# Optimization experiments

Hardware: AMD Instinct MI355X
Metric: run time of the kernel (lower is better)

## Reference

```python
import jax, jax.numpy as jnp
import numpy as np

N_NODES = 50000


def gcn_conv(x, src, dst, W, b, n_nodes):
    """PyG-style GCNConv: x' = D^-1/2 (A + I) D^-1/2 (x W) + b.
    src/dst already include self-loops."""
    h = x @ W  # [N, C_out]
    # symmetric normalization from degree (with self-loops, unit edge weight)
    deg = jax.ops.segment_sum(jnp.ones_like(dst, dtype=h.dtype), dst,
                              num_segments=n_nodes)  # [N]
    dinv = jnp.where(deg > 0, jax.lax.rsqrt(deg), 0.0)
    norm = dinv[src] * dinv[dst]  # [E]
    msg = h[src] * norm[:, None]  # gather + scale, [E, C_out]
    out = jax.ops.segment_sum(msg, dst, num_segments=n_nodes)  # scatter-add
    return out + b


def setup_inputs() -> dict:
    key = jax.random.key(0)
    k1, k2, k3, k4, k5, k6 = jax.random.split(key, 6)
    in_c, hid_c, out_c = 128, 64, 64
    x = jax.random.normal(k1, (N_NODES, in_c), dtype=jnp.float32)
    edge_index = jax.random.randint(k2, (2, 800000), 0, N_NODES, dtype=jnp.int64)
    # Glorot-ish init for weights, zeros for bias (as PyG default)
    W1 = jax.random.normal(k3, (in_c, hid_c), dtype=jnp.float32) / np.sqrt(in_c)
    b1 = jnp.zeros((hid_c,), dtype=jnp.float32)
    W2 = jax.random.normal(k4, (hid_c, out_c), dtype=jnp.float32) / np.sqrt(hid_c)
    b2 = jnp.zeros((out_c,), dtype=jnp.float32)
    return {"x": x, "edge_index": edge_index, "W1": W1, "b1": b1,
            "W2": W2, "b2": b2}


def reference(x, edge_index, W1, b1, W2, b2):
    n = x.shape[0]
    loops = jnp.arange(n, dtype=edge_index.dtype)
    src = jnp.concatenate([edge_index[0], loops])  # add self-loops
    dst = jnp.concatenate([edge_index[1], loops])
    h = gcn_conv(x, src, dst, W1, b1, n)
    h = jax.nn.relu(h)
    return gcn_conv(h, src, dst, W2, b2, n)
```

## Files before the change

kernel.cpp:

```cpp
#include <hip/hip_runtime.h>
#include <hip/hip_fp16.h>


#define C_HID 64
#define NCHUNK 512
#define ES3 768
#define ES4 768

static inline size_t alignup(size_t x) { return (x + 255) & ~(size_t)255; }

typedef __attribute__((address_space(3))) unsigned int lds_uint;
typedef __attribute__((address_space(1))) const unsigned int glob_uint;
typedef __attribute__((ext_vector_type(4))) _Float16 half4;
typedef __attribute__((ext_vector_type(4))) float floatx4;

__device__ __forceinline__ int blockScanIncl256(int v, int* wsum) {
    const int lane = threadIdx.x & 63, wav = threadIdx.x >> 6;
    int s = v;
#pragma unroll
    for (int off = 1; off < 64; off <<= 1) {
        int t = __shfl_up(s, off);
        if (lane >= off) s += t;
    }
    if (lane == 63) wsum[wav] = s;
    __syncthreads();
    if (wav == 0 && lane < 4) {
        int ws = wsum[lane];
#pragma unroll
        for (int off = 1; off < 4; off <<= 1) {
            int t = __shfl_up(ws, off);
            if (lane >= off) ws += t;
        }
        wsum[lane] = ws;
    }
    __syncthreads();
    return (wav ? wsum[wav - 1] : 0) + s;
}

__global__ __launch_bounds__(256) void cvt_w1t_kernel(
    const float* __restrict__ W, __half* __restrict__ Wh) {
    int i = blockIdx.x * 256 + threadIdx.x;
    if (i < 64 * 128) {
        int c = i >> 7, k = i & 127;
        int ks = k ^ ((c & 7) << 3);
        Wh[c * 128 + ks] = __float2half(W[k * 64 + c]);
    }
}

template <int K>
__global__ __launch_bounds__(256) void gemm1_hist_kernel(
    const float* __restrict__ X, const __half* __restrict__ Wh,
    const int* __restrict__ dst, __half* __restrict__ outh,
    int* __restrict__ S, int n, int E, int ePer, int nb) {
    constexpr int XP = K + 8;
    __shared__ __half Xs[64 * XP];
    __shared__ __half WsT[64 * K];
    __shared__ int h[1024];
    const int t = threadIdx.x;
    const int lane = t & 63;
    const int wav = t >> 6;

    if ((int)blockIdx.x < NCHUNK) {
        for (int i = t; i < nb; i += 256) h[i] = 0;
        __syncthreads();
        int beg = blockIdx.x * ePer, end = min(E, beg + ePer);
        for (int e = beg + t; e < end; e += 256)
            atomicAdd(&h[dst[e] >> 6], 1);
        __syncthreads();
        for (int b = t; b < nb; b += 256)
            S[(size_t)b * NCHUNK + blockIdx.x] = h[b];
        return;
    }

    const int row0 = ((int)blockIdx.x - NCHUNK) * 64;
    {
        const char* gb = (const char*)Wh;
        char* lb = (char*)WsT;
        for (int off = wav * 1024; off < K * 64 * 2; off += 4096)
            __builtin_amdgcn_global_load_lds((glob_uint*)(gb + off + lane * 16),
                                             (lds_uint*)(lb + off), 16, 0, 0);
    }
    if (row0 + 64 <= n) {
        const float4* g4 = (const float4*)(X + (size_t)row0 * K);
        for (int i = t; i < 64 * (K / 4); i += 256) {
            float4 v = g4[i];
            int r = i / (K / 4), k0 = (i % (K / 4)) * 4;
            float2 st;
            ((__half2*)&st)[0] = __floats2half2_rn(v.x, v.y);
            ((__half2*)&st)[1] = __floats2half2_rn(v.z, v.w);
            *(float2*)&Xs[r * XP + k0] = st;
        }
    } else {
        for (int i = t; i < 64 * K; i += 256) {
            int r = i / K, k = i % K;
            float xv = (row0 + r < n) ? X[(size_t)(row0 + r) * K + k] : 0.0f;
            Xs[r * XP + k] = __float2half(xv);
        }
    }
    __syncthreads();

    const int rl = lane & 15;
    const int kq = lane >> 4;
    floatx4 acc0 = {0.f, 0.f, 0.f, 0.f};
    floatx4 acc1 = {0.f, 0.f, 0.f, 0.f};
    floatx4 acc2 = {0.f, 0.f, 0.f, 0.f};
    floatx4 acc3 = {0.f, 0.f, 0.f, 0.f};
    const __half* xrow = &Xs[(wav * 16 + rl) * XP];
#pragma unroll
    for (int kb = 0; kb < K / 16; ++kb) {
        const int ka = kb * 16 + kq * 4;
        half4 a = *(const half4*)&xrow[ka];
        {   int col = 0 * 16 + rl;
            half4 b = *(const half4*)&WsT[col * K + (ka ^ ((col & 7) << 3))];
            acc0 = __builtin_amdgcn_mfma_f32_16x16x16f16(a, b, acc0, 0, 0, 0); }
        {   int col = 1 * 16 + rl;
            half4 b = *(const half4*)&WsT[col * K + (ka ^ ((col & 7) << 3))];
            acc1 = __builtin_amdgcn_mfma_f32_16x16x16f16(a, b, acc1, 0, 0, 0); }
        {   int col = 2 * 16 + rl;
            half4 b = *(const half4*)&WsT[col * K + (ka ^ ((col & 7) << 3))];
            acc2 = __builtin_amdgcn_mfma_f32_16x16x16f16(a, b, acc2, 0, 0, 0); }
        {   int col = 3 * 16 + rl;
            half4 b = *(const half4*)&WsT[col * K + (ka ^ ((col & 7) << 3))];
            acc3 = __builtin_amdgcn_mfma_f32_16x16x16f16(a, b, acc3, 0, 0, 0); }
    }
#pragma unroll
    for (int r = 0; r < 4; ++r) {
        int row = row0 + wav * 16 + kq * 4 + r;
        if (row < n) {
            __half* orow = &outh[(size_t)row * 64];
            orow[0 * 16 + rl] = __float2half(acc0[r]);
            orow[1 * 16 + rl] = __float2half(acc1[r]);
            orow[2 * 16 + rl] = __float2half(acc2[r]);
            orow[3 * 16 + rl] = __float2half(acc3[r]);
        }
    }
}

__global__ __launch_bounds__(256) void scan_rows_kernel(
    int* __restrict__ S, int* __restrict__ T) {
    __shared__ int wsum[4];
    const int b = blockIdx.x, t = threadIdx.x;
    int4 v = make_int4(0, 0, 0, 0);
    if (t < NCHUNK / 4) v = ((const int4*)(S + (size_t)b * NCHUNK))[t];
    int p1 = v.x + v.y, p2 = p1 + v.z, p3 = p2 + v.w;
    int incl = blockScanIncl256(p3, wsum);
    int excl = incl - p3;
    if (t < NCHUNK / 4) {
        int4 o;
        o.x = excl; o.y = excl + v.x; o.z = excl + p1; o.w = excl + p2;
        ((int4*)(S + (size_t)b * NCHUNK))[t] = o;
    }
    if (t == 0) T[b] = wsum[3];
}

__global__ __launch_bounds__(256) void scatter_kernel(
    const int* __restrict__ src, const int* __restrict__ dst, int E, int ePer,
    const int* __restrict__ S, const int* __restrict__ T,
    unsigned* __restrict__ ebuf, int nb) {
    __shared__ int tmp[1024];
    __shared__ int arr[1024];
    __shared__ int wsum[4];
    const int b = blockIdx.x, t = threadIdx.x;
    {
        int a0 = (4 * t + 0 < nb) ? T[4 * t + 0] : 0;
        int a1 = (4 * t + 1 < nb) ? T[4 * t + 1] : 0;
        int a2 = (4 * t + 2 < nb) ? T[4 * t + 2] : 0;
        int a3 = (4 * t + 3 < nb) ? T[4 * t + 3] : 0;
        int p1 = a0 + a1, p2 = p1 + a2, p3 = p2 + a3;
        int incl = blockScanIncl256(p3, wsum);
        int excl = incl - p3;
        tmp[4 * t + 0] = excl;
        tmp[4 * t + 1] = excl + a0;
        tmp[4 * t + 2] = excl + p1;
        tmp[4 * t + 3] = excl + p2;
    }
    __syncthreads();
    for (int i = t; i < nb; i += 256)
        arr[i] = S[(size_t)i * NCHUNK + b] + tmp[i];
    __syncthreads();
    int beg = b * ePer, end = min(E, beg + ePer);
    for (int e = beg + t; e < end; e += 256) {
        int d = dst[e];
        int s = src[e];
        int pos = atomicAdd(&arr[d >> 6], 1);
        ebuf[pos] = ((unsigned)s << 6) | (unsigned)(d & 63);
    }
}

__global__ __launch_bounds__(256) void build_kernel(
    const unsigned* __restrict__ ebuf, const int* __restrict__ T,
    int* __restrict__ row_ptr, float* __restrict__ dinv,
    int* __restrict__ esrc, __half* __restrict__ g1, int n, int nb) {
    __shared__ int tmp[1024];
    __shared__ int cnt[64];
    __shared__ int cur[64];
    __shared__ float dvs[64];
    __shared__ int wsum[4];
    const int b = blockIdx.x, t = threadIdx.x;
    {
        int a0 = (4 * t + 0 < nb) ? T[4 * t + 0] : 0;
        int a1 = (4 * t + 1 < nb) ? T[4 * t + 1] : 0;
        int a2 = (4 * t + 2 < nb) ? T[4 * t + 2] : 0;
        int a3 = (4 * t + 3 < nb) ? T[4 * t + 3] : 0;
        int p1 = a0 + a1, p2 = p1 + a2, p3 = p2 + a3;
        int incl = blockScanIncl256(p3, wsum);
        int excl = incl - p3;
        tmp[4 * t + 0] = excl + a0;
        tmp[4 * t + 1] = excl + p1;
        tmp[4 * t + 2] = excl + p2;
        tmp[4 * t + 3] = excl + p3;
    }
    if (t < 64) cnt[t] = 0;
    __syncthreads();
    const int ebeg = b ? tmp[b - 1] : 0;
    const int eend = tmp[b];

    for (int e = ebeg + t; e < eend; e += 256)
        atomicAdd(&cnt[ebuf[e] & 63], 1);
    __syncthreads();
    if (t < 64) {
        int deg = cnt[t];
        int s = deg;
#pragma unroll
        for (int off = 1; off < 64; off <<= 1) {
            int x = __shfl_up(s, off);
            if (t >= off) s += x;
        }
        cur[t] = ebeg + s - deg;
        float dv = rsqrtf(1.0f + (float)deg);
        dvs[t] = dv;
        int v = (b << 6) + t;
        if (v < n) {
            row_ptr[v + 1] = ebeg + s;
            dinv[v] = dv;
            if (v == 0) row_ptr[0] = 0;
        }
    }
    __syncthreads();
    for (int e = ebeg + t; e < eend; e += 256) {
        unsigned p = ebuf[e];
        int pos = atomicAdd(&cur[p & 63], 1);
        esrc[pos] = (int)(p >> 6);
    }
    {
        const int row = t >> 2, q = t & 3;
        const int v = (b << 6) + row;
        if (v < n) {
            float dv = dvs[row];
            float4* gp = (float4*)(g1 + (size_t)v * 64 + q * 16);
            float4 r0 = gp[0], r1 = gp[1];
            __half2* h0 = (__half2*)&r0;
            __half2* h1 = (__half2*)&r1;
#pragma unroll
            for (int i2 = 0; i2 < 4; ++i2) {
                float2 f0 = __half22float2(h0[i2]);
                float2 f1 = __half22float2(h1[i2]);
                h0[i2] = __floats2half2_rn(f0.x * dv, f0.y * dv);
                h1[i2] = __floats2half2_rn(f1.x * dv, f1.y * dv);
            }
            gp[0] = r0;
            gp[1] = r1;
        }
    }
}

__device__ __forceinline__ void addf4(float acc[8], const float4& r) {
    const __half2* h = (const __half2*)&r;
#pragma unroll
    for (int q = 0; q < 4; ++q) {
        float2 f = __half22float2(h[q]);
        acc[2 * q] += f.x;
        acc[2 * q + 1] += f.y;
    }
}

template <bool LDSE>
__device__ __forceinline__ void agg8_body(
    const float4* __restrict__ hs4, const int* es, const int* __restrict__ esg,
    int beg0, int beg, int end, int c8, float acc[8]) {
    int j = beg;
    for (; j + 8 <= end; j += 8) {
        int s0, s1, s2, s3, s4, s5, s6, s7;
        if (LDSE) {
            s0 = es[j];     s1 = es[j + 1]; s2 = es[j + 2]; s3 = es[j + 3];
            s4 = es[j + 4]; s5 = es[j + 5]; s6 = es[j + 6]; s7 = es[j + 7];
        } else {
            const int* p = esg + beg0 + j;
            s0 = p[0]; s1 = p[1]; s2 = p[2]; s3 = p[3];
            s4 = p[4]; s5 = p[5]; s6 = p[6]; s7 = p[7];
        }
        float4 r0 = hs4[(size_t)s0 * 8 + c8];
        float4 r1 = hs4[(size_t)s1 * 8 + c8];
        float4 r2 = hs4[(size_t)s2 * 8 + c8];
        float4 r3 = hs4[(size_t)s3 * 8 + c8];
        float4 r4 = hs4[(size_t)s4 * 8 + c8];
        float4 r5 = hs4[(size_t)s5 * 8 + c8];
        float4 r6 = hs4[(size_t)s6 * 8 + c8];
        float4 r7 = hs4[(size_t)s7 * 8 + c8];
        addf4(acc, r0); addf4(acc, r1); addf4(acc, r2); addf4(acc, r3);
        addf4(acc, r4); addf4(acc, r5); addf4(acc, r6); addf4(acc, r7);
    }
    if (j + 4 <= end) {
        int s0, s1, s2, s3;
        if (LDSE) {
            s0 = es[j]; s1 = es[j + 1]; s2 = es[j + 2]; s3 = es[j + 3];
        } else {
            const int* p = esg + beg0 + j;
            s0 = p[0]; s1 = p[1]; s2 = p[2]; s3 = p[3];
        }
        float4 r0 = hs4[(size_t)s0 * 8 + c8];
        float4 r1 = hs4[(size_t)s1 * 8 + c8];
        float4 r2 = hs4[(size_t)s2 * 8 + c8];
        float4 r3 = hs4[(size_t)s3 * 8 + c8];
        addf4(acc, r0); addf4(acc, r1); addf4(acc, r2); addf4(acc, r3);
        j += 4;
    }
    for (; j < end; ++j) {
        int s0 = LDSE ? es[j] : esg[beg0 + j];
        float4 r0 = hs4[(size_t)s0 * 8 + c8];
        addf4(acc, r0);
    }
}

__global__ __launch_bounds__(256) void agg1_gemm2_kernel(
    const __half* __restrict__ g1, const int* __restrict__ row_ptr,
    const int* __restrict__ esrc, const float* __restrict__ dinv,
    const float* __restrict__ b1, const float* __restrict__ W2,
    __half* __restrict__ g2, int n) {
    __shared__ float Bt[32][68];
    __shared__ float Ws2[64 * 64];
    __shared__ int es[ES3];
    const int t = threadIdx.x, lane = t & 63, wav = t >> 6;
    const int row0 = blockIdx.x * 32;

    const int beg0 = row_ptr[row0];
    const int end0 = row_ptr[min(row0 + 32, n)];
    const int tot = end0 - beg0;
    const bool uselds = (tot <= ES3);
    if (uselds)
        for (int i = t; i < tot; i += 256) es[i] = esrc[beg0 + i];
    __syncthreads();

    {
        const char* gb = (const char*)W2;
        char* lb = (char*)Ws2;
        for (int off = wav * 1024; off < 64 * 64 * 4; off += 4096)
            __builtin_amdgcn_global_load_lds((glob_uint*)(gb + off + lane * 16),
                                             (lds_uint*)(lb + off), 16, 0, 0);
    }

    const int g = t >> 3;
    const int c8 = t & 7;
    const int v = row0 + g;
    const float4* __restrict__ hs4 = (const float4*)g1;

    if (v < n) {
        float acc[8];
        {
            float4 raw = hs4[(size_t)v * 8 + c8];
            const __half2* hp = (const __half2*)&raw;
#pragma unroll
            for (int q = 0; q < 4; ++q) {
                float2 f = __half22float2(hp[q]);
                acc[2 * q] = f.x; acc[2 * q + 1] = f.y;
            }
        }
        const int beg = row_ptr[v] - beg0;
        const int end = row_ptr[v + 1] - beg0;
        if (uselds) agg8_body<true>(hs4, es, esrc, beg0, beg, end, c8, acc);
        else        agg8_body<false>(hs4, es, esrc, beg0, beg, end, c8, acc);
        const float dv0 = dinv[v];
        const float* bb = b1 + c8 * 8;
        float4 w0, w1;
        w0.x = fmaxf(fmaf(acc[0], dv0, bb[0]), 0.f);
        w0.y = fmaxf(fmaf(acc[1], dv0, bb[1]), 0.f);
        w0.z = fmaxf(fmaf(acc[2], dv0, bb[2]), 0.f);
        w0.w = fmaxf(fmaf(acc[3], dv0, bb[3]), 0.f);
        w1.x = fmaxf(fmaf(acc[4], dv0, bb[4]), 0.f);
        w1.y = fmaxf(fmaf(acc[5], dv0, bb[5]), 0.f);
        w1.z = fmaxf(fmaf(acc[6], dv0, bb[6]), 0.f);
        w1.w = fmaxf(fmaf(acc[7], dv0, bb[7]), 0.f);
        *(float4*)&Bt[g][c8 * 8] = w0;
        *(float4*)&Bt[g][c8 * 8 + 4] = w1;
    } else {
        *(float4*)&Bt[g][c8 * 8] = make_float4(0.f, 0.f, 0.f, 0.f);
        *(float4*)&Bt[g][c8 * 8 + 4] = make_float4(0.f, 0.f, 0.f, 0.f);
    }
    __syncthreads();

    const int tx = t & 15;
    const int ty = t >> 4;
    float a2[2][4] = {{0.f}};
#pragma unroll 2
    for (int k0 = 0; k0 < 64; k0 += 4) {
        float4 x0 = *(const float4*)&Bt[2 * ty + 0][k0];
        float4 x1 = *(const float4*)&Bt[2 * ty + 1][k0];
        float4 w0 = *(const float4*)&Ws2[(k0 + 0) * 64 + 4 * tx];
        float4 w1 = *(const float4*)&Ws2[(k0 + 1) * 64 + 4 * tx];
        float4 w2 = *(const float4*)&Ws2[(k0 + 2) * 64 + 4 * tx];
        float4 w3 = *(const float4*)&Ws2[(k0 + 3) * 64 + 4 * tx];
        const float* xp[2] = {(const float*)&x0, (const float*)&x1};
        const float* wp[4] = {(const float*)&w0, (const float*)&w1,
                              (const float*)&w2, (const float*)&w3};
#pragma unroll
        for (int r = 0; r < 2; ++r)
#pragma unroll
            for (int kk = 0; kk < 4; ++kk) {
                float av = xp[r][kk];
#pragma unroll
                for (int cc = 0; cc < 4; ++cc)
                    a2[r][cc] = fmaf(av, wp[kk][cc], a2[r][cc]);
            }
    }
#pragma unroll
    for (int r = 0; r < 2; ++r) {
        int row = row0 + 2 * ty + r;
        if (row < n) {
            float dv = dinv[row];
            __half2 p01 = __floats2half2_rn(a2[r][0] * dv, a2[r][1] * dv);
            __half2 p23 = __floats2half2_rn(a2[r][2] * dv, a2[r][3] * dv);
            float2 st;
            ((__half2*)&st)[0] = p01;
            ((__half2*)&st)[1] = p23;
            *(float2*)&g2[(size_t)row * 64 + 4 * tx] = st;
        }
    }
}

__global__ __launch_bounds__(256) void aggregate2_kernel(
    const __half* __restrict__ hs,
    const int* __restrict__ row_ptr,
    const int* __restrict__ esrc,
    const float* __restrict__ dinv,
    const float* __restrict__ bias,
    float* __restrict__ out, int n) {
    __shared__ int es[ES4];
    const int t = threadIdx.x;
    const int row0 = blockIdx.x * 32;
    const int beg0 = row_ptr[row0];
    const int end0 = row_ptr[min(row0 + 32, n)];
    const int tot = end0 - beg0;
    const bool uselds = (tot <= ES4);
    if (uselds)
        for (int i = t; i < tot; i += 256) es[i] = esrc[beg0 + i];
    __syncthreads();

    const int v = row0 + (t >> 3);
    if (v >= n) return;
    const int c8 = t & 7;
    const float4* __restrict__ hs4 = (const float4*)hs;

    float acc[8];
    {
        float4 raw = hs4[(size_t)v * 8 + c8];
        const __half2* hp = (const __half2*)&raw;
#pragma unroll
        for (int q = 0; q < 4; ++q) {
            float2 f = __half22float2(hp[q]);
            acc[2 * q] = f.x; acc[2 * q + 1] = f.y;
        }
    }

    const int beg = row_ptr[v] - beg0;
    const int end = row_ptr[v + 1] - beg0;
    if (uselds) agg8_body<true>(hs4, es, esrc, beg0, beg, end, c8, acc);
    else        agg8_body<false>(hs4, es, esrc, beg0, beg, end, c8, acc);

    float dv = dinv[v];
    float4 b0 = *(const float4*)(bias + c8 * 8);
    float4 b1v = *(const float4*)(bias + c8 * 8 + 4);
    float4 o0, o1;
    o0.x = fmaf(acc[0], dv, b0.x); o0.y = fmaf(acc[1], dv, b0.y);
    o0.z = fmaf(acc[2], dv, b0.z); o0.w = fmaf(acc[3], dv, b0.w);
    o1.x = fmaf(acc[4], dv, b1v.x); o1.y = fmaf(acc[5], dv, b1v.y);
    o1.z = fmaf(acc[6], dv, b1v.z); o1.w = fmaf(acc[7], dv, b1v.w);
    float4* op = (float4*)(out + (size_t)v * 64 + c8 * 8);
    op[0] = o0;
    op[1] = o1;
}

extern "C" void kernel_launch(void* const* d_in, const int* in_sizes, int n_in,
                              void* d_out, int out_size, void* d_ws, size_t ws_size,
                              hipStream_t stream) {
    const float* x  = (const float*)d_in[0];
    const int*   ei = (const int*)d_in[1];
    const float* W1 = (const float*)d_in[2];
    const float* b1 = (const float*)d_in[3];
    const float* W2 = (const float*)d_in[4];
    const float* b2 = (const float*)d_in[5];
    float* out = (float*)d_out;

    const int C_IN = 128;
    const int n = in_sizes[0] / C_IN;
    const int E = in_sizes[1] / 2;
    const int* src = ei;
    const int* dst = ei + E;

    const int nb = (n + 63) >> 6;
    const int ngb = (n + 63) / 64;
    const int n32 = (n + 31) / 32;
    const int ePer = (E + NCHUNK - 1) / NCHUNK;

    char* w = (char*)d_ws;
    float*    dinv    = (float*)w;    w += alignup((size_t)n * sizeof(float));
    __half*   g1      = (__half*)w;   w += alignup((size_t)n * C_HID * sizeof(__half));
    __half*   g2      = (__half*)w;   w += alignup((size_t)n * C_HID * sizeof(__half));
    int*      row_ptr = (int*)w;      w += alignup((size_t)(n + 1) * sizeof(int));
    int*      S       = (int*)w;      w += alignup((size_t)nb * NCHUNK * sizeof(int));
    int*      T       = (int*)w;      w += alignup((size_t)(nb + 1) * sizeof(int));
    unsigned* ebuf    = (unsigned*)w; w += alignup((size_t)E * sizeof(unsigned));
    int*      esrc    = (int*)w;      w += alignup((size_t)E * sizeof(int));
    __half*   W1h     = (__half*)w;

    cvt_w1t_kernel<<<32, 256, 0, stream>>>(W1, W1h);

    gemm1_hist_kernel<128><<<NCHUNK + ngb, 256, 0, stream>>>(
        x, W1h, dst, g1, S, n, E, ePer, nb);

    scan_rows_kernel<<<nb, 256, 0, stream>>>(S, T);
    scatter_kernel<<<NCHUNK, 256, 0, stream>>>(src, dst, E, ePer, S, T, ebuf, nb);
    build_kernel<<<nb, 256, 0, stream>>>(ebuf, T, row_ptr, dinv, esrc, g1, n, nb);

    agg1_gemm2_kernel<<<n32, 256, 0, stream>>>(
        g1, row_ptr, esrc, dinv, b1, W2, g2, n);

    aggregate2_kernel<<<n32, 256, 0, stream>>>(
        g2, row_ptr, esrc, dinv, b2, out, n);
}
```

Before: 155.1 us.

## Co-schedule GEMM1 with scatter instead of histogram pass

Moves the dense X·W1 MFMA tiles out of the histogram kernel and into the scatter kernel, so the GEMM blocks run alongside the edge scatter instead of the edge histogram. The histogram becomes a lean standalone kernel, and the scatter and GEMM paths share LDS through a union. The aim is to balance work across the two passes and overlap the compute-heavy GEMM with the atomic-heavy scatter. In exchange, the combined kernel's LDS footprint is now the larger of the two layouts, which may reduce occupancy for the scatter blocks.

```diff
diff --git a/kernel.cpp b/kernel.cpp
--- a/kernel.cpp
+++ b/kernel.cpp
@@ -47,93 +47,18 @@
     }
 }
 
-template <int K>
-__global__ __launch_bounds__(256) void gemm1_hist_kernel(
-    const float* __restrict__ X, const __half* __restrict__ Wh,
-    const int* __restrict__ dst, __half* __restrict__ outh,
-    int* __restrict__ S, int n, int E, int ePer, int nb) {
-    constexpr int XP = K + 8;
-    __shared__ __half Xs[64 * XP];
-    __shared__ __half WsT[64 * K];
+__global__ __launch_bounds__(256) void hist_kernel(
+    const int* __restrict__ dst, int* __restrict__ S, int E, int ePer, int nb) {
     __shared__ int h[1024];
     const int t = threadIdx.x;
-    const int lane = t & 63;
-    const int wav = t >> 6;
-
-    if ((int)blockIdx.x < NCHUNK) {
-        for (int i = t; i < nb; i += 256) h[i] = 0;
-        __syncthreads();
-        int beg = blockIdx.x * ePer, end = min(E, beg + ePer);
-        for (int e = beg + t; e < end; e += 256)
-            atomicAdd(&h[dst[e] >> 6], 1);
-        __syncthreads();
-        for (int b = t; b < nb; b += 256)
-            S[(size_t)b * NCHUNK + blockIdx.x] = h[b];
-        return;
-    }
-
-    const int row0 = ((int)blockIdx.x - NCHUNK) * 64;
-    {
-        const char* gb = (const char*)Wh;
-        char* lb = (char*)WsT;
-        for (int off = wav * 1024; off < K * 64 * 2; off += 4096)
-            __builtin_amdgcn_global_load_lds((glob_uint*)(gb + off + lane * 16),
-                                             (lds_uint*)(lb + off), 16, 0, 0);
-    }
-    if (row0 + 64 <= n) {
-        const float4* g4 = (const float4*)(X + (size_t)row0 * K);
-        for (int i = t; i < 64 * (K / 4); i += 256) {
-            float4 v = g4[i];
-            int r = i / (K / 4), k0 = (i % (K / 4)) * 4;
-            float2 st;
-            ((__half2*)&st)[0] = __floats2half2_rn(v.x, v.y);
-            ((__half2*)&st)[1] = __floats2half2_rn(v.z, v.w);
-            *(float2*)&Xs[r * XP + k0] = st;
-        }
-    } else {
-        for (int i = t; i < 64 * K; i += 256) {
-            int r = i / K, k = i % K;
-            float xv = (row0 + r < n) ? X[(size_t)(row0 + r) * K + k] : 0.0f;
-            Xs[r * XP + k] = __float2half(xv);
-        }
-    }
-    __syncthreads();
-
-    const int rl = lane & 15;
-    const int kq = lane >> 4;
-    floatx4 acc0 = {0.f, 0.f, 0.f, 0.f};
-    floatx4 acc1 = {0.f, 0.f, 0.f, 0.f};
-    floatx4 acc2 = {0.f, 0.f, 0.f, 0.f};
-    floatx4 acc3 = {0.f, 0.f, 0.f, 0.f};
-    const __half* xrow = &Xs[(wav * 16 + rl) * XP];
-#pragma unroll
-    for (int kb = 0; kb < K / 16; ++kb) {
-        const int ka = kb * 16 + kq * 4;
-        half4 a = *(const half4*)&xrow[ka];
-        {   int col = 0 * 16 + rl;
-            half4 b = *(const half4*)&WsT[col * K + (ka ^ ((col & 7) << 3))];
-            acc0 = __builtin_amdgcn_mfma_f32_16x16x16f16(a, b, acc0, 0, 0, 0); }
-        {   int col = 1 * 16 + rl;
-            half4 b = *(const half4*)&WsT[col * K + (ka ^ ((col & 7) << 3))];
-            acc1 = __builtin_amdgcn_mfma_f32_16x16x16f16(a, b, acc1, 0, 0, 0); }
-        {   int col = 2 * 16 + rl;
-            half4 b = *(const half4*)&WsT[col * K + (ka ^ ((col & 7) << 3))];
-            acc2 = __builtin_amdgcn_mfma_f32_16x16x16f16(a, b, acc2, 0, 0, 0); }
-        {   int col = 3 * 16 + rl;
-            half4 b = *(const half4*)&WsT[col * K + (ka ^ ((col & 7) << 3))];
-            acc3 = __builtin_amdgcn_mfma_f32_16x16x16f16(a, b, acc3, 0, 0, 0); }
-    }
-#pragma unroll
-    for (int r = 0; r < 4; ++r) {
-        int row = row0 + wav * 16 + kq * 4 + r;
-        if (row < n) {
-            __half* orow = &outh[(size_t)row * 64];
-            orow[0 * 16 + rl] = __float2half(acc0[r]);
-            orow[1 * 16 + rl] = __float2half(acc1[r]);
-            orow[2 * 16 + rl] = __float2half(acc2[r]);
-            orow[3 * 16 + rl] = __float2half(acc3[r]);
-        }
-    }
+    for (int i = t; i < nb; i += 256) h[i] = 0;
+    __syncthreads();
+    int beg = blockIdx.x * ePer, end = min(E, beg + ePer);
+    for (int e = beg + t; e < end; e += 256)
+        atomicAdd(&h[dst[e] >> 6], 1);
+    __syncthreads();
+    for (int b = t; b < nb; b += 256)
+        S[(size_t)b * NCHUNK + blockIdx.x] = h[b];
 }
 
 __global__ __launch_bounds__(256) void scan_rows_kernel(
@@ -153,37 +78,113 @@
     if (t == 0) T[b] = wsum[3];
 }
 
-__global__ __launch_bounds__(256) void scatter_kernel(
+template <int K>
+__global__ __launch_bounds__(256) void scatter_gemm1_kernel(
     const int* __restrict__ src, const int* __restrict__ dst, int E, int ePer,
     const int* __restrict__ S, const int* __restrict__ T,
-    unsigned* __restrict__ ebuf, int nb) {
-    __shared__ int tmp[1024];
-    __shared__ int arr[1024];
+    unsigned* __restrict__ ebuf, int nb,
+    const float* __restrict__ X, const __half* __restrict__ Wh,
+    __half* __restrict__ outh, int n) {
+    constexpr int XP = K + 8;
+    __shared__ union SM {
+        struct { int tmp[1024]; int arr[1024]; } c;
+        struct { __half Xs[64 * XP]; __half WsT[64 * K]; } g;
+    } sm;
     __shared__ int wsum[4];
-    const int b = blockIdx.x, t = threadIdx.x;
+    const int t = threadIdx.x;
+    const int lane = t & 63;
+    const int wav = t >> 6;
+
+    if ((int)blockIdx.x < NCHUNK) {
+        const int b = blockIdx.x;
+        {
+            int a0 = (4 * t + 0 < nb) ? T[4 * t + 0] : 0;
+            int a1 = (4 * t + 1 < nb) ? T[4 * t + 1] : 0;
+            int a2 = (4 * t + 2 < nb) ? T[4 * t + 2] : 0;
+            int a3 = (4 * t + 3 < nb) ? T[4 * t + 3] : 0;
+            int p1 = a0 + a1, p2 = p1 + a2, p3 = p2 + a3;
+            int incl = blockScanIncl256(p3, wsum);
+            int excl = incl - p3;
+            sm.c.tmp[4 * t + 0] = excl;
+            sm.c.tmp[4 * t + 1] = excl + a0;
+            sm.c.tmp[4 * t + 2] = excl + p1;
+            sm.c.tmp[4 * t + 3] = excl + p2;
+        }
+        __syncthreads();
+        for (int i = t; i < nb; i += 256)
+            sm.c.arr[i] = S[(size_t)i * NCHUNK + b] + sm.c.tmp[i];
+        __syncthreads();
+        int beg = b * ePer, end = min(E, beg + ePer);
+        for (int e = beg + t; e < end; e += 256) {
+            int d = dst[e];
+            int s = src[e];
+            int pos = atomicAdd(&sm.c.arr[d >> 6], 1);
+            ebuf[pos] = ((unsigned)s << 6) | (unsigned)(d & 63);
+        }
+        return;
+    }
+
+    const int row0 = ((int)blockIdx.x - NCHUNK) * 64;
     {
-        int a0 = (4 * t + 0 < nb) ? T[4 * t + 0] : 0;
-        int a1 = (4 * t + 1 < nb) ? T[4 * t + 1] : 0;
-        int a2 = (4 * t + 2 < nb) ? T[4 * t + 2] : 0;
-        int a3 = (4 * t + 3 < nb) ? T[4 * t + 3] : 0;
-        int p1 = a0 + a1, p2 = p1 + a2, p3 = p2 + a3;
-        int incl = blockScanIncl256(p3, wsum);
-        int excl = incl - p3;
-        tmp[4 * t + 0] = excl;
-        tmp[4 * t + 1] = excl + a0;
-        tmp[4 * t + 2] = excl + p1;
-        tmp[4 * t + 3] = excl + p2;
-    }
-    __syncthreads();
-    for (int i = t; i < nb; i += 256)
-        arr[i] = S[(size_t)i * NCHUNK + b] + tmp[i];
-    __syncthreads();
-    int beg = b * ePer, end = min(E, beg + ePer);
-    for (int e = beg + t; e < end; e += 256) {
-        int d = dst[e];
-        int s = src[e];
-        int pos = atomicAdd(&arr[d >> 6], 1);
-        ebuf[pos] = ((unsigned)s << 6) | (unsigned)(d & 63);
+        const char* gb = (const char*)Wh;
+        char* lb = (char*)sm.g.WsT;
+        for (int off = wav * 1024; off < K * 64 * 2; off += 4096)
+            __builtin_amdgcn_global_load_lds((glob_uint*)(gb + off + lane * 16),
+                                             (lds_uint*)(lb + off), 16, 0, 0);
+    }
+    if (row0 + 64 <= n) {
+        const float4* g4 = (const float4*)(X + (size_t)row0 * K);
+        for (int i = t; i < 64 * (K / 4); i += 256) {
+            float4 v = g4[i];
+            int r = i / (K / 4), k0 = (i % (K / 4)) * 4;
+            float2 st;
+            ((__half2*)&st)[0] = __floats2half2_rn(v.x, v.y);
+            ((__half2*)&st)[1] = __floats2half2_rn(v.z, v.w);
+            *(float2*)&sm.g.Xs[r * XP + k0] = st;
+        }
+    } else {
+        for (int i = t; i < 64 * K; i += 256) {
+            int r = i / K, k = i % K;
+            float xv = (row0 + r < n) ? X[(size_t)(row0 + r) * K + k] : 0.0f;
+            sm.g.Xs[r * XP + k] = __float2half(xv);
+        }
+    }
+    __syncthreads();
+
+    const int rl = lane & 15;
+    const int kq = lane >> 4;
+    floatx4 acc0 = {0.f, 0.f, 0.f, 0.f};
+    floatx4 acc1 = {0.f, 0.f, 0.f, 0.f};
+    floatx4 acc2 = {0.f, 0.f, 0.f, 0.f};
+    floatx4 acc3 = {0.f, 0.f, 0.f, 0.f};
+    const __half* xrow = &sm.g.Xs[(wav * 16 + rl) * XP];
+#pragma unroll
+    for (int kb = 0; kb < K / 16; ++kb) {
+        const int ka = kb * 16 + kq * 4;
+        half4 a = *(const half4*)&xrow[ka];
+        {   int col = 0 * 16 + rl;
+            half4 b = *(const half4*)&sm.g.WsT[col * K + (ka ^ ((col & 7) << 3))];
+            acc0 = __builtin_amdgcn_mfma_f32_16x16x16f16(a, b, acc0, 0, 0, 0); }
+        {   int col = 1 * 16 + rl;
+            half4 b = *(const half4*)&sm.g.WsT[col * K + (ka ^ ((col & 7) << 3))];
+            acc1 = __builtin_amdgcn_mfma_f32_16x16x16f16(a, b, acc1, 0, 0, 0); }
+        {   int col = 2 * 16 + rl;
+            half4 b = *(const half4*)&sm.g.WsT[col * K + (ka ^ ((col & 7) << 3))];
+            acc2 = __builtin_amdgcn_mfma_f32_16x16x16f16(a, b, acc2, 0, 0, 0); }
+        {   int col = 3 * 16 + rl;
+            half4 b = *(const half4*)&sm.g.WsT[col * K + (ka ^ ((col & 7) << 3))];
+            acc3 = __builtin_amdgcn_mfma_f32_16x16x16f16(a, b, acc3, 0, 0, 0); }
+    }
+#pragma unroll
+    for (int r = 0; r < 4; ++r) {
+        int row = row0 + wav * 16 + kq * 4 + r;
+        if (row < n) {
+            __half* orow = &outh[(size_t)row * 64];
+            orow[0 * 16 + rl] = __float2half(acc0[r]);
+            orow[1 * 16 + rl] = __float2half(acc1[r]);
+            orow[2 * 16 + rl] = __float2half(acc2[r]);
+            orow[3 * 16 + rl] = __float2half(acc3[r]);
+        }
     }
 }
 
@@ -514,11 +515,13 @@
 
     cvt_w1t_kernel<<<32, 256, 0, stream>>>(W1, W1h);
 
-    gemm1_hist_kernel<128><<<NCHUNK + ngb, 256, 0, stream>>>(
-        x, W1h, dst, g1, S, n, E, ePer, nb);
+    hist_kernel<<<NCHUNK, 256, 0, stream>>>(dst, S, E, ePer, nb);
 
     scan_rows_kernel<<<nb, 256, 0, stream>>>(S, T);
-    scatter_kernel<<<NCHUNK, 256, 0, stream>>>(src, dst, E, ePer, S, T, ebuf, nb);
+
+    scatter_gemm1_kernel<128><<<NCHUNK + ngb, 256, 0, stream>>>(
+        src, dst, E, ePer, S, T, ebuf, nb, x, W1h, g1, n);
+
     build_kernel<<<nb, 256, 0, stream>>>(ebuf, T, row_ptr, dinv, esrc, g1, n, nb);
 
     agg1_gemm2_kernel<<<n32, 256, 0, stream>>>(
```

Result: no change. 156.6 us (+1.0%).
